# Optimization experiments

Hardware: AMD Instinct MI355X
Metric: run time of the kernel (lower is better)

## Reference

```python
import jax, jax.numpy as jnp
import numpy as np

B, S, E, D, H, L, V = 8, 128, 512, 1024, 16, 4, 32000
DH = D // H
FF = 4 * D
SCALE = 1.0 / (DH ** 0.5)
NEG = -1e30


def _layer_norm(x, g, b, eps=1e-5):
    m = jnp.mean(x, axis=-1, keepdims=True)
    v = jnp.mean((x - m) ** 2, axis=-1, keepdims=True)
    return (x - m) / jnp.sqrt(v + eps) * g + b


def _rel_shift(x):
    # x: [q, k, b, n] -> TransformerXL relative shift
    q, k, b, n = x.shape
    xp = jnp.concatenate([jnp.zeros((q, 1, b, n), x.dtype), x], axis=1)
    xp = xp.reshape(k + 1, q, b, n)
    return xp[1:].reshape(q, k, b, n)


def setup_inputs():
    key = jax.random.key(0)
    ks = jax.random.split(key, 40)
    g = lambda i, shape, s=0.02: jax.random.normal(ks[i], shape, jnp.float32) * s
    inp = {
        'input_ids': jax.random.randint(ks[0], (B, E), 0, V),
        'encoder_rep': jax.random.normal(ks[1], (B, E, D), jnp.float32),
        'input_mask': jnp.ones((B, E), jnp.float32),
        'decode_input': jax.random.randint(ks[2], (B, S), 0, V),
        'decode_target': jax.random.randint(ks[3], (B, S), 0, V),
        'word_emb': g(4, (V, D)),
        'qkv_w': g(5, (L, 3 * D, D)), 'r_w': g(6, (L, D, D)), 'o_w': g(7, (L, D, D)),
        'kv_w': g(8, (L, 2 * D, D)), 'q_w': g(9, (L, D, D)), 'io_w': g(10, (L, D, D)),
        'rr_bias': g(11, (L, H, DH)), 'rw_bias': g(12, (L, H, DH)),
        'ln1_g': jnp.ones((L, D)), 'ln1_b': jnp.zeros((L, D)),
        'ln2_g': jnp.ones((L, D)), 'ln2_b': jnp.zeros((L, D)),
        'ffn_w1': g(13, (L, FF, D)), 'ffn_b1': jnp.zeros((L, FF)),
        'ffn_w2': g(14, (L, D, FF)), 'ffn_b2': jnp.zeros((L, D)),
        'ln3_g': jnp.ones((L, D)), 'ln3_b': jnp.zeros((L, D)),
        'out_w': g(15, (D, D)), 'out_b': jnp.zeros((D,)),
        'copy_w': g(16, (D, D)), 'copy_b': jnp.zeros((D,)),
        'mode_w': g(17, (1, D)), 'mode_b': jnp.zeros((1,)),
    }
    return inp


def _forward(input_ids, encoder_rep, input_mask, decode_input, decode_target,
             word_emb, qkv_w, r_w, o_w, kv_w, q_w, io_w, rr_bias, rw_bias,
             ln1_g, ln1_b, ln2_g, ln2_b, ffn_w1, ffn_b1, ffn_w2, ffn_b2,
             ln3_g, ln3_b, out_w, out_b, copy_w, copy_b, mode_w, mode_b):
    # relative position embedding r: [S, D]
    pos_seq = jnp.arange(S - 1, -1, -1.0, dtype=jnp.float32)
    inv_freq = 1.0 / (10000.0 ** (jnp.arange(0.0, D, 2.0) / D))
    sin_inp = pos_seq[:, None] * inv_freq[None, :]
    r = jnp.concatenate([jnp.sin(sin_inp), jnp.cos(sin_inp)], axis=-1)

    causal = jnp.tril(jnp.ones((S, S), jnp.bool_))[:, :, None, None]  # [i,j,1,1]
    enc_mask_t = input_mask.T  # [E, B]

    core = word_emb[decode_input].transpose(1, 0, 2)  # [S, B, D]
    enc_t = encoder_rep.transpose(1, 0, 2)            # [E, B, D]

    for l in range(L):
        w = core
        heads = w @ qkv_w[l].T  # [S,B,3D]
        q, k, v = jnp.split(heads, 3, axis=-1)
        q = q.reshape(S, B, H, DH); k = k.reshape(S, B, H, DH); v = v.reshape(S, B, H, DH)
        r_k = (r @ r_w[l].T).reshape(S, H, DH)
        AC = jnp.einsum('ibnd,jbnd->ijbn', q + rw_bias[l], k)
        BD = _rel_shift(jnp.einsum('ibnd,jnd->ijbn', q + rr_bias[l], r_k))
        score = (AC + BD) * SCALE
        score = jnp.where(causal, score, NEG)
        prob = jax.nn.softmax(score, axis=1)
        vec = jnp.einsum('ijbn,jbnd->ibnd', prob, v).reshape(S, B, D)
        x = _layer_norm(w + vec @ o_w[l].T, ln1_g[l], ln1_b[l])

        # cross attention
        kv = enc_t @ kv_w[l].T
        k2, v2 = jnp.split(kv, 2, axis=-1)
        k2 = k2.reshape(E, B, H, DH); v2 = v2.reshape(E, B, H, DH)
        q2 = (x @ q_w[l].T).reshape(S, B, H, DH)
        score2 = jnp.einsum('qbnd,kbnd->qkbn', q2, k2) * SCALE
        score2 = score2 + (1.0 - enc_mask_t)[None, :, :, None] * NEG
        prob2 = jax.nn.softmax(score2, axis=1)
        vec2 = jnp.einsum('ijbn,jbnd->ibnd', prob2, v2).reshape(S, B, D)
        y = _layer_norm(x + vec2 @ io_w[l].T, ln2_g[l], ln2_b[l])

        # FFN (exact GELU as torch nn.GELU default)
        h = jax.nn.gelu(y @ ffn_w1[l].T + ffn_b1[l], approximate=False)
        h = h @ ffn_w2[l].T + ffn_b2[l]
        core = _layer_norm(y + h, ln3_g[l], ln3_b[l])

    core_out = core.transpose(1, 0, 2)  # [B, S, D]
    output = core_out @ out_w.T + out_b
    vocab_logits = output @ word_emb.T  # [B,S,V]
    vocab_prob = jax.nn.softmax(vocab_logits, axis=-1)

    copy_h = core_out @ copy_w.T + copy_b
    input_logits = jnp.einsum('bid,bjd->bij', copy_h, encoder_rep)
    input_logits = input_logits + (1.0 - input_mask[:, None, :]) * NEG
    input_prob = jax.nn.softmax(input_logits, axis=-1)  # [B,S,E]

    mode_sig = jax.nn.sigmoid(core_out @ mode_w.T + mode_b)  # [B,S,1]
    vocab_prob = vocab_prob * mode_sig

    idx = jnp.broadcast_to(input_ids[:, None, :], (B, S, E))
    b_i = jnp.arange(B)[:, None, None]
    s_i = jnp.arange(S)[None, :, None]
    vocab_prob = vocab_prob.at[b_i, s_i, idx].add((1.0 - mode_sig) * input_prob)

    flat = vocab_prob.reshape(-1, V)
    tgt = decode_target.reshape(-1)
    predict = jnp.take_along_axis(flat, tgt[:, None], axis=1)[:, 0]
    valid = (tgt != 0).astype(jnp.float32)
    loss = jnp.sum(-jnp.log(predict + 1e-6) * valid) / jnp.sum(valid)
    return jnp.repeat(loss[None], B)


def reference(input_ids, encoder_rep, input_mask, decode_input, decode_target,
              word_emb, qkv_w, r_w, o_w, kv_w, q_w, io_w, rr_bias, rw_bias,
              ln1_g, ln1_b, ln2_g, ln2_b, ffn_w1, ffn_b1, ffn_w2, ffn_b2,
              ln3_g, ln3_b, out_w, out_b, copy_w, copy_b, mode_w, mode_b):
    return _forward(input_ids, encoder_rep, input_mask, decode_input, decode_target,
                    word_emb, qkv_w, r_w, o_w, kv_w, q_w, io_w, rr_bias, rw_bias,
                    ln1_g, ln1_b, ln2_g, ln2_b, ffn_w1, ffn_b1, ffn_w2, ffn_b2,
                    ln3_g, ln3_b, out_w, out_b, copy_w, copy_b, mode_w, mode_b)
```

## Files before the change

kernel.cpp:

```cpp
#include <hip/hip_runtime.h>
#include <math.h>

#define B_ 8
#define S_ 128
#define E_ 512
#define D_ 1024
#define H_ 16
#define L_ 4
#define V_ 32000
#define DH_ 64
#define FF_ 4096
#define M_ 1024
#define ME_ 4096
#define NT_ 250
#define SCALE_F 0.125f
#define NEGV (-1e30f)

typedef __attribute__((ext_vector_type(8))) short short8;
typedef __attribute__((ext_vector_type(4))) float f32x4;

__device__ __forceinline__ float bf2f(ushort u) {
  union { unsigned int u32; float f; } v; v.u32 = ((unsigned int)u) << 16; return v.f;
}
__device__ __forceinline__ ushort f2bf(float x) {
  union { float f; unsigned int u; } v; v.f = x;
  unsigned int r = v.u + 0x7fff + ((v.u >> 16) & 1);
  return (ushort)(r >> 16);
}
__device__ __forceinline__ void gl_lds16(const ushort* g, ushort* l) {
  __builtin_amdgcn_global_load_lds((const __attribute__((address_space(1))) void*)g,
                                   (__attribute__((address_space(3))) void*)l, 16, 0, 0);
}

__device__ __forceinline__ float warp_reduce_sum(float v) {
#pragma unroll
  for (int o = 32; o > 0; o >>= 1) v += __shfl_down(v, o);
  return v;
}
__device__ __forceinline__ float warp_reduce_max(float v) {
#pragma unroll
  for (int o = 32; o > 0; o >>= 1) v = fmaxf(v, __shfl_down(v, o));
  return v;
}
__device__ __forceinline__ float block_reduce_sum(float v, float* sred) {
  v = warp_reduce_sum(v);
  __syncthreads();
  if ((threadIdx.x & 63) == 0) sred[threadIdx.x >> 6] = v;
  __syncthreads();
  float s = 0.0f;
  int nw = blockDim.x >> 6;
  for (int w = 0; w < nw; ++w) s += sred[w];
  return s;
}
__device__ __forceinline__ float block_reduce_max(float v, float* sred) {
  v = warp_reduce_max(v);
  __syncthreads();
  if ((threadIdx.x & 63) == 0) sred[threadIdx.x >> 6] = v;
  __syncthreads();
  float s = -3.4e38f;
  int nw = blockDim.x >> 6;
  for (int w = 0; w < nw; ++w) s = fmaxf(s, sred[w]);
  return s;
}

__global__ __launch_bounds__(256) void castf_kernel(const float* __restrict__ in,
                                                    ushort* __restrict__ out, int n4) {
  int t = blockIdx.x * 256 + threadIdx.x;
  if (t >= n4) return;
  float4 v = ((const float4*)in)[t];
  ushort4 o;
  o.x = f2bf(v.x); o.y = f2bf(v.y); o.z = f2bf(v.z); o.w = f2bf(v.w);
  ((ushort4*)out)[t] = o;
}

__global__ __launch_bounds__(256) void castlayer_kernel(
    const float* __restrict__ sqkv, const float* __restrict__ so,
    const float* __restrict__ sq, const float* __restrict__ sio,
    const float* __restrict__ sf1, const float* __restrict__ sf2,
    ushort* __restrict__ dqkv, ushort* __restrict__ dov,
    ushort* __restrict__ dq, ushort* __restrict__ dio,
    ushort* __restrict__ df1, ushort* __restrict__ df2) {
  int t = blockIdx.x * 256 + threadIdx.x;
  const float* src; ushort* dst; int idx;
  if (t < 786432)       { src = sqkv; dst = dqkv; idx = t; }
  else if (t < 1048576) { src = so;  dst = dov; idx = t - 786432; }
  else if (t < 1310720) { src = sq;  dst = dq;  idx = t - 1048576; }
  else if (t < 1572864) { src = sio; dst = dio; idx = t - 1310720; }
  else if (t < 2621440) { src = sf1; dst = df1; idx = t - 1572864; }
  else if (t < 3670016) { src = sf2; dst = df2; idx = t - 2621440; }
  else return;
  float4 v = ((const float4*)src)[idx];
  ushort4 o4;
  o4.x = f2bf(v.x); o4.y = f2bf(v.y); o4.z = f2bf(v.z); o4.w = f2bf(v.w);
  ((ushort4*)dst)[idx] = o4;
}

__global__ __launch_bounds__(256) void enct_kernel(const float* __restrict__ enc,
                                                   ushort* __restrict__ encT) {
  int t = blockIdx.x * 256 + threadIdx.x;
  if (t >= ME_ * D_) return;
  int d = t & (D_ - 1);
  int row = t >> 10;
  int e = row >> 3, b = row & 7;
  encT[t] = f2bf(enc[((size_t)b * E_ + e) * D_ + d]);
}

__global__ __launch_bounds__(256) void pos_emb_kernel(ushort* __restrict__ r) {
  int t = blockIdx.x * 256 + threadIdx.x;
  if (t >= S_ * D_) return;
  int i = t / D_, j = t % D_;
  float pos = (float)(S_ - 1 - i);
  int jj = (j < D_ / 2) ? j : (j - D_ / 2);
  float invf = powf(10000.0f, -(float)(2 * jj) / (float)D_);
  float a = pos * invf;
  r[t] = f2bf((j < D_ / 2) ? sinf(a) : cosf(a));
}

__global__ __launch_bounds__(256) void embed_kernel(const int* __restrict__ ids,
                                                    const float* __restrict__ emb,
                                                    float* __restrict__ core,
                                                    ushort* __restrict__ core_bf) {
  int t = blockIdx.x * 256 + threadIdx.x;
  if (t >= M_ * D_) return;
  int d = t & (D_ - 1);
  int row = t >> 10;
  int s = row >> 3, b = row & 7;
  float v = emb[(size_t)ids[b * S_ + s] * D_ + d];
  core[t] = v;
  core_bf[t] = f2bf(v);
}

template <int EPI>
__global__ __launch_bounds__(256) void gemm_w_kernel(
    const ushort* __restrict__ A, const ushort* __restrict__ Bm,
    const float* __restrict__ bias, void* __restrict__ Cv,
    int M, int N, int K, int ksplit,
    long long Arow, long long Abatch, long long Brow, long long Bbatch,
    long long Crow, long long Cbatch, long long Csplit) {
  __shared__ ushort lA[128 * 32];
  __shared__ ushort lB[128 * 32];
  int tid = threadIdx.x;
  int bz = blockIdx.z;
  int batch = bz / ksplit, split = bz % ksplit;
  int kLen = K / ksplit, kStart = split * kLen;
  const ushort* Ab = A + (size_t)batch * Abatch;
  const ushort* Bb = Bm + (size_t)batch * Bbatch;
  int bm = blockIdx.y * 128, bn = blockIdx.x * 128;
  int lane = tid & 63, wave = tid >> 6;
  int wrow = (wave >> 1) * 64, wcol = (wave & 1) * 64;
  int quad = lane >> 4, l16 = lane & 15;
  f32x4 acc[4][4];
#pragma unroll
  for (int i = 0; i < 4; ++i)
#pragma unroll
    for (int j = 0; j < 4; ++j) { acc[i][j][0] = 0.f; acc[i][j][1] = 0.f; acc[i][j][2] = 0.f; acc[i][j][3] = 0.f; }
  int r0 = tid >> 2, c0 = (tid & 3) * 8;
  int r1 = (tid + 256) >> 2;
  for (int k0 = kStart; k0 < kStart + kLen; k0 += 32) {
    __syncthreads();
    gl_lds16(Ab + (size_t)(bm + r0) * Arow + k0 + c0, &lA[(size_t)tid * 8]);
    gl_lds16(Ab + (size_t)(bm + r1) * Arow + k0 + c0, &lA[(size_t)(256 + tid) * 8]);
    gl_lds16(Bb + (size_t)(bn + r0) * Brow + k0 + c0, &lB[(size_t)tid * 8]);
    gl_lds16(Bb + (size_t)(bn + r1) * Brow + k0 + c0, &lB[(size_t)(256 + tid) * 8]);
    __syncthreads();
    short8 af[4], bfr[4];
#pragma unroll
    for (int mi = 0; mi < 4; ++mi)
      af[mi] = *(const short8*)&lA[(size_t)(wrow + mi * 16 + l16) * 32 + quad * 8];
#pragma unroll
    for (int ni = 0; ni < 4; ++ni)
      bfr[ni] = *(const short8*)&lB[(size_t)(wcol + ni * 16 + l16) * 32 + quad * 8];
#pragma unroll
    for (int mi = 0; mi < 4; ++mi)
#pragma unroll
      for (int ni = 0; ni < 4; ++ni)
        acc[mi][ni] = __builtin_amdgcn_mfma_f32_16x16x32_bf16(af[mi], bfr[ni], acc[mi][ni], 0, 0, 0);
  }
#pragma unroll
  for (int mi = 0; mi < 4; ++mi) {
    int row0 = bm + wrow + mi * 16 + quad * 4;
#pragma unroll
    for (int ni = 0; ni < 4; ++ni) {
      int col = bn + wcol + ni * 16 + l16;
      float bv = 0.f;
      if (EPI >= 3) bv = bias[col];
#pragma unroll
      for (int r = 0; r < 4; ++r) {
        float v = acc[mi][ni][r] + bv;
        if (EPI == 4) v = 0.5f * v * (1.0f + erff(v * 0.70710678118654752f));
        size_t ci = (size_t)split * Csplit + (size_t)batch * Cbatch + (size_t)(row0 + r) * Crow + col;
        if (EPI == 0) ((float*)Cv)[ci] = v;
        else ((ushort*)Cv)[ci] = f2bf(v);
      }
    }
  }
}

__global__ __launch_bounds__(256) void vocab_kernel(const ushort* __restrict__ A,
                                                    const ushort* __restrict__ Bm,
                                                    float* __restrict__ tmax,
                                                    float* __restrict__ tsum) {
  __shared__ ushort lA[128 * 32];
  __shared__ ushort lB[128 * 32];
  __shared__ float smax[2][128];
  __shared__ float ssum[2][128];
  int tid = threadIdx.x;
  int orig = blockIdx.x + gridDim.x * blockIdx.y;
  int wg = (orig & 7) * 250 + (orig >> 3);
  int bm = (wg & 7) * 128;
  int bnT = wg >> 3;
  int bn = bnT * 128;
  int lane = tid & 63, wave = tid >> 6;
  int wrow = (wave >> 1) * 64, half = wave & 1, wcol = half * 64;
  int quad = lane >> 4, l16 = lane & 15;
  f32x4 acc[4][4];
#pragma unroll
  for (int i = 0; i < 4; ++i)
#pragma unroll
    for (int j = 0; j < 4; ++j) { acc[i][j][0] = 0.f; acc[i][j][1] = 0.f; acc[i][j][2] = 0.f; acc[i][j][3] = 0.f; }
  int r0 = tid >> 2, c0 = (tid & 3) * 8;
  int r1 = (tid + 256) >> 2;
  for (int k0 = 0; k0 < D_; k0 += 32) {
    __syncthreads();
    gl_lds16(A + (size_t)(bm + r0) * 2048 + k0 + c0, &lA[(size_t)tid * 8]);
    gl_lds16(A + (size_t)(bm + r1) * 2048 + k0 + c0, &lA[(size_t)(256 + tid) * 8]);
    gl_lds16(Bm + (size_t)(bn + r0) * D_ + k0 + c0, &lB[(size_t)tid * 8]);
    gl_lds16(Bm + (size_t)(bn + r1) * D_ + k0 + c0, &lB[(size_t)(256 + tid) * 8]);
    __syncthreads();
    short8 af[4], bfr[4];
#pragma unroll
    for (int mi = 0; mi < 4; ++mi)
      af[mi] = *(const short8*)&lA[(size_t)(wrow + mi * 16 + l16) * 32 + quad * 8];
#pragma unroll
    for (int ni = 0; ni < 4; ++ni)
      bfr[ni] = *(const short8*)&lB[(size_t)(wcol + ni * 16 + l16) * 32 + quad * 8];
#pragma unroll
    for (int mi = 0; mi < 4; ++mi)
#pragma unroll
      for (int ni = 0; ni < 4; ++ni)
        acc[mi][ni] = __builtin_amdgcn_mfma_f32_16x16x32_bf16(af[mi], bfr[ni], acc[mi][ni], 0, 0, 0);
  }
#pragma unroll
  for (int mi = 0; mi < 4; ++mi)
#pragma unroll
    for (int r = 0; r < 4; ++r) {
      float lm = -3.4e38f;
#pragma unroll
      for (int ni = 0; ni < 4; ++ni) lm = fmaxf(lm, acc[mi][ni][r]);
#pragma unroll
      for (int o = 1; o < 16; o <<= 1) lm = fmaxf(lm, __shfl_xor(lm, o));
      if (l16 == 0) smax[half][wrow + mi * 16 + quad * 4 + r] = lm;
    }
  __syncthreads();
#pragma unroll
  for (int mi = 0; mi < 4; ++mi)
#pragma unroll
    for (int r = 0; r < 4; ++r) {
      int row = wrow + mi * 16 + quad * 4 + r;
      float m = fmaxf(smax[0][row], smax[1][row]);
      float ls = 0.f;
#pragma unroll
      for (int ni = 0; ni < 4; ++ni) ls += __expf(acc[mi][ni][r] - m);
#pragma unroll
      for (int o = 1; o < 16; o <<= 1) ls += __shfl_xor(ls, o);
      if (l16 == 0) ssum[half][row] = ls;
    }
  __syncthreads();
  if (tid < 128) {
    float m = fmaxf(smax[0][tid], smax[1][tid]);
    float s = ssum[0][tid] + ssum[1][tid];
    tmax[(size_t)(bm + tid) * NT_ + bnT] = m;
    tsum[(size_t)(bm + tid) * NT_ + bnT] = s;
  }
}

__global__ __launch_bounds__(256) void vocab_combine_kernel(const float* __restrict__ tmax,
                                                            const float* __restrict__ tsum,
                                                            float* __restrict__ rmax,
                                                            float* __restrict__ rsum) {
  __shared__ float sred[4];
  int m = blockIdx.x;
  float mx = -3.4e38f;
  for (int t = threadIdx.x; t < NT_; t += 256) mx = fmaxf(mx, tmax[(size_t)m * NT_ + t]);
  mx = block_reduce_max(mx, sred);
  float s = 0.f;
  for (int t = threadIdx.x; t < NT_; t += 256)
    s += tsum[(size_t)m * NT_ + t] * expf(tmax[(size_t)m * NT_ + t] - mx);
  s = block_reduce_sum(s, sred);
  if (threadIdx.x == 0) { rmax[m] = mx; rsum[m] = s; }
}

__global__ __launch_bounds__(256) void tlogit_kernel(const ushort* __restrict__ headout,
                                                     const ushort* __restrict__ emb,
                                                     const int* __restrict__ tgt,
                                                     float* __restrict__ tl) {
  __shared__ float sred[4];
  int m = blockIdx.x;
  int s = m >> 3, b = m & 7;
  int t = tgt[b * S_ + s];
  const ushort* a = headout + (size_t)m * 2048;
  const ushort* w = emb + (size_t)t * D_;
  float acc = 0.f;
  for (int i = threadIdx.x; i < D_; i += 256) acc += bf2f(a[i]) * bf2f(w[i]);
  acc = block_reduce_sum(acc, sred);
  if (threadIdx.x == 0) tl[m] = acc;
}

__global__ __launch_bounds__(256) void attn1_fused_kernel(const ushort* __restrict__ heads,
                                                          const ushort* __restrict__ rkproj,
                                                          const float* __restrict__ rw,
                                                          const float* __restrict__ rr,
                                                          ushort* __restrict__ attnA) {
  __shared__ float score[128][129];
  __shared__ ushort pP[128][136];
  __shared__ ushort vT[64][136];
  int bz = blockIdx.x;
  int b = bz >> 4, n = bz & 15;
  int tid = threadIdx.x, lane = tid & 63, wave = tid >> 6;
  int quad = lane >> 4, l16 = lane & 15;
  int wrow = wave * 32;

  {
    int j = tid >> 1, dbase = (tid & 1) * 32;
    const ushort* src = heads + (size_t)(j * 8 + b) * 3072 + 2048 + n * 64 + dbase;
#pragma unroll
    for (int c8 = 0; c8 < 4; ++c8) {
      short8 v8 = *(const short8*)(src + c8 * 8);
#pragma unroll
      for (int cc = 0; cc < 8; ++cc) vT[dbase + c8 * 8 + cc][j] = (ushort)v8[cc];
    }
  }

  short8 qrw[2][2], qrr[2][2];
#pragma unroll
  for (int mi = 0; mi < 2; ++mi) {
    int i = wrow + mi * 16 + l16;
    const ushort* qp = heads + (size_t)(i * 8 + b) * 3072 + n * 64;
#pragma unroll
    for (int kc = 0; kc < 2; ++kc) {
      int k0 = kc * 32 + quad * 8;
      short8 qv = *(const short8*)(qp + k0);
      short8 w, rv;
#pragma unroll
      for (int t = 0; t < 8; ++t) {
        float q = bf2f((ushort)qv[t]);
        w[t] = (short)f2bf(q + rw[n * 64 + k0 + t]);
        rv[t] = (short)f2bf(q + rr[n * 64 + k0 + t]);
      }
      qrw[mi][kc] = w; qrr[mi][kc] = rv;
    }
  }

  {
    f32x4 acc[2][8];
#pragma unroll
    for (int i = 0; i < 2; ++i)
#pragma unroll
      for (int j = 0; j < 8; ++j) { acc[i][j][0]=0.f; acc[i][j][1]=0.f; acc[i][j][2]=0.f; acc[i][j][3]=0.f; }
#pragma unroll
    for (int kc = 0; kc < 2; ++kc) {
      int k0 = kc * 32 + quad * 8;
      short8 kf[8];
#pragma unroll
      for (int ni = 0; ni < 8; ++ni) {
        int j = ni * 16 + l16;
        kf[ni] = *(const short8*)(heads + (size_t)(j * 8 + b) * 3072 + 1024 + n * 64 + k0);
      }
#pragma unroll
      for (int mi = 0; mi < 2; ++mi)
#pragma unroll
        for (int ni = 0; ni < 8; ++ni)
          acc[mi][ni] = __builtin_amdgcn_mfma_f32_16x16x32_bf16(qrw[mi][kc], kf[ni], acc[mi][ni], 0, 0, 0);
    }
#pragma unroll
    for (int mi = 0; mi < 2; ++mi)
#pragma unroll
      for (int ni = 0; ni < 8; ++ni)
#pragma unroll
        for (int r = 0; r < 4; ++r)
          score[wrow + mi * 16 + quad * 4 + r][ni * 16 + l16] = acc[mi][ni][r];
  }
  {
    f32x4 acc[2][8];
#pragma unroll
    for (int i = 0; i < 2; ++i)
#pragma unroll
      for (int j = 0; j < 8; ++j) { acc[i][j][0]=0.f; acc[i][j][1]=0.f; acc[i][j][2]=0.f; acc[i][j][3]=0.f; }
#pragma unroll
    for (int kc = 0; kc < 2; ++kc) {
      int k0 = kc * 32 + quad * 8;
      short8 rkf[8];
#pragma unroll
      for (int ni = 0; ni < 8; ++ni) {
        int jp = ni * 16 + l16;
        rkf[ni] = *(const short8*)(rkproj + (size_t)jp * 1024 + n * 64 + k0);
      }
#pragma unroll
      for (int mi = 0; mi < 2; ++mi)
#pragma unroll
        for (int ni = 0; ni < 8; ++ni)
          acc[mi][ni] = __builtin_amdgcn_mfma_f32_16x16x32_bf16(qrr[mi][kc], rkf[ni], acc[mi][ni], 0, 0, 0);
    }
#pragma unroll
    for (int mi = 0; mi < 2; ++mi)
#pragma unroll
      for (int r = 0; r < 4; ++r) {
        int i = wrow + mi * 16 + quad * 4 + r;
#pragma unroll
        for (int ni = 0; ni < 8; ++ni) {
          int jp = ni * 16 + l16;
          if (jp >= 127 - i) score[i][jp - 127 + i] += acc[mi][ni][r];
        }
      }
  }
  {
    int row = tid >> 1, halfc = (tid & 1) * 64;
    float mx = -3.4e38f;
    for (int c = halfc; c < halfc + 64; ++c) {
      float v = (c <= row) ? score[row][c] * SCALE_F : -3.4e38f;
      mx = fmaxf(mx, v);
    }
    mx = fmaxf(mx, __shfl_xor(mx, 1));
    float s = 0.f;
    for (int c = halfc; c < halfc + 64; ++c) {
      float e = (c <= row) ? __expf(score[row][c] * SCALE_F - mx) : 0.f;
      score[row][c] = e;
      s += e;
    }
    s += __shfl_xor(s, 1);
    float inv = 1.0f / s;
    for (int c = halfc; c < halfc + 64; ++c) pP[row][c] = f2bf(score[row][c] * inv);
  }
  __syncthreads();
  {
    f32x4 acc[2][4];
#pragma unroll
    for (int i = 0; i < 2; ++i)
#pragma unroll
      for (int j = 0; j < 4; ++j) { acc[i][j][0]=0.f; acc[i][j][1]=0.f; acc[i][j][2]=0.f; acc[i][j][3]=0.f; }
#pragma unroll
    for (int kc = 0; kc < 4; ++kc) {
      int k0 = kc * 32 + quad * 8;
      short8 pf[2], vf[4];
#pragma unroll
      for (int mi = 0; mi < 2; ++mi)
        pf[mi] = *(const short8*)&pP[wrow + mi * 16 + l16][k0];
#pragma unroll
      for (int ni = 0; ni < 4; ++ni)
        vf[ni] = *(const short8*)&vT[ni * 16 + l16][k0];
#pragma unroll
      for (int mi = 0; mi < 2; ++mi)
#pragma unroll
        for (int ni = 0; ni < 4; ++ni)
          acc[mi][ni] = __builtin_amdgcn_mfma_f32_16x16x32_bf16(pf[mi], vf[ni], acc[mi][ni], 0, 0, 0);
    }
#pragma unroll
    for (int mi = 0; mi < 2; ++mi)
#pragma unroll
      for (int r = 0; r < 4; ++r) {
        int i = wrow + mi * 16 + quad * 4 + r;
#pragma unroll
        for (int ni = 0; ni < 4; ++ni)
          attnA[(size_t)(i * 8 + b) * 1024 + n * 64 + ni * 16 + l16] = f2bf(acc[mi][ni][r]);
      }
  }
}

__global__ __launch_bounds__(256) void attn2_fused_kernel(const float* __restrict__ q0,
                                                          const float* __restrict__ q1,
                                                          const ushort* __restrict__ kvproj,
                                                          const float* __restrict__ mask,
                                                          ushort* __restrict__ attnA) {
  __shared__ ushort vT[64][136];
  __shared__ ushort pP[128][136];
  __shared__ float mtile[128];
  int bz = blockIdx.x;
  int b = bz >> 4, n = bz & 15;
  int tid = threadIdx.x, lane = tid & 63, wave = tid >> 6;
  int quad = lane >> 4, l16 = lane & 15;
  int wrow = wave * 32;
  short8 qf[2][2];
#pragma unroll
  for (int mi = 0; mi < 2; ++mi) {
    int i = wrow + mi * 16 + l16;
    size_t base = (size_t)(i * 8 + b) * 1024 + n * 64;
#pragma unroll
    for (int kc = 0; kc < 2; ++kc) {
      int k0 = kc * 32 + quad * 8;
      short8 v;
#pragma unroll
      for (int t = 0; t < 8; ++t) v[t] = (short)f2bf(q0[base + k0 + t] + q1[base + k0 + t]);
      qf[mi][kc] = v;
    }
  }
  float m_run[2][4], l_run[2][4];
#pragma unroll
  for (int mi = 0; mi < 2; ++mi)
#pragma unroll
    for (int r = 0; r < 4; ++r) { m_run[mi][r] = -3.0e38f; l_run[mi][r] = 0.f; }
  f32x4 accO[2][4];
#pragma unroll
  for (int i = 0; i < 2; ++i)
#pragma unroll
    for (int j = 0; j < 4; ++j) { accO[i][j][0]=0.f; accO[i][j][1]=0.f; accO[i][j][2]=0.f; accO[i][j][3]=0.f; }

  for (int et = 0; et < 4; ++et) {
    __syncthreads();
    {
      int j = tid >> 1, dbase = (tid & 1) * 32;
      int e = et * 128 + j;
      const ushort* src = kvproj + (size_t)(e * 8 + b) * 2048 + 1024 + n * 64 + dbase;
#pragma unroll
      for (int c8 = 0; c8 < 4; ++c8) {
        short8 v8 = *(const short8*)(src + c8 * 8);
#pragma unroll
        for (int cc = 0; cc < 8; ++cc) vT[dbase + c8 * 8 + cc][j] = (ushort)v8[cc];
      }
      if (tid < 128) mtile[tid] = (1.0f - mask[b * E_ + et * 128 + tid]) * NEGV;
    }
    f32x4 accS[2][8];
#pragma unroll
    for (int i = 0; i < 2; ++i)
#pragma unroll
      for (int j = 0; j < 8; ++j) { accS[i][j][0]=0.f; accS[i][j][1]=0.f; accS[i][j][2]=0.f; accS[i][j][3]=0.f; }
#pragma unroll
    for (int kc = 0; kc < 2; ++kc) {
      int k0 = kc * 32 + quad * 8;
      short8 kf[8];
#pragma unroll
      for (int ni = 0; ni < 8; ++ni) {
        int e = et * 128 + ni * 16 + l16;
        kf[ni] = *(const short8*)(kvproj + (size_t)(e * 8 + b) * 2048 + n * 64 + k0);
      }
#pragma unroll
      for (int mi = 0; mi < 2; ++mi)
#pragma unroll
        for (int ni = 0; ni < 8; ++ni)
          accS[mi][ni] = __builtin_amdgcn_mfma_f32_16x16x32_bf16(qf[mi][kc], kf[ni], accS[mi][ni], 0, 0, 0);
    }
    __syncthreads();
#pragma unroll
    for (int mi = 0; mi < 2; ++mi)
#pragma unroll
      for (int r = 0; r < 4; ++r) {
        float v[8];
        float vmax = -3.4e38f;
#pragma unroll
        for (int ni = 0; ni < 8; ++ni) {
          v[ni] = accS[mi][ni][r] * SCALE_F + mtile[ni * 16 + l16];
          vmax = fmaxf(vmax, v[ni]);
        }
#pragma unroll
        for (int o = 1; o < 16; o <<= 1) vmax = fmaxf(vmax, __shfl_xor(vmax, o));
        float mnew = fmaxf(m_run[mi][r], vmax);
        float alpha = __expf(m_run[mi][r] - mnew);
        float ls = 0.f;
        int row = wrow + mi * 16 + quad * 4 + r;
#pragma unroll
        for (int ni = 0; ni < 8; ++ni) {
          float p = __expf(v[ni] - mnew);
          ls += p;
          pP[row][ni * 16 + l16] = f2bf(p);
        }
#pragma unroll
        for (int o = 1; o < 16; o <<= 1) ls += __shfl_xor(ls, o);
        l_run[mi][r] = l_run[mi][r] * alpha + ls;
        m_run[mi][r] = mnew;
#pragma unroll
        for (int ni = 0; ni < 4; ++ni) accO[mi][ni][r] *= alpha;
      }
#pragma unroll
    for (int kc = 0; kc < 4; ++kc) {
      int k0 = kc * 32 + quad * 8;
      short8 pf[2], vf[4];
#pragma unroll
      for (int mi = 0; mi < 2; ++mi)
        pf[mi] = *(const short8*)&pP[wrow + mi * 16 + l16][k0];
#pragma unroll
      for (int ni = 0; ni < 4; ++ni)
        vf[ni] = *(const short8*)&vT[ni * 16 + l16][k0];
#pragma unroll
      for (int mi = 0; mi < 2; ++mi)
#pragma unroll
        for (int ni = 0; ni < 4; ++ni)
          accO[mi][ni] = __builtin_amdgcn_mfma_f32_16x16x32_bf16(pf[mi], vf[ni], accO[mi][ni], 0, 0, 0);
    }
  }
#pragma unroll
  for (int mi = 0; mi < 2; ++mi)
#pragma unroll
    for (int r = 0; r < 4; ++r) {
      int i = wrow + mi * 16 + quad * 4 + r;
      float inv = 1.0f / l_run[mi][r];
#pragma unroll
      for (int ni = 0; ni < 4; ++ni)
        attnA[(size_t)(i * 8 + b) * 1024 + n * 64 + ni * 16 + l16] = f2bf(accO[mi][ni][r] * inv);
    }
}

__global__ __launch_bounds__(256) void addln_kernel(const float* __restrict__ a,
                                                    const float* __restrict__ c,
                                                    int nsplit, long long cstride,
                                                    const float* __restrict__ bias,
                                                    const float* __restrict__ g,
                                                    const float* __restrict__ bb,
                                                    float* __restrict__ out,
                                                    ushort* __restrict__ out_bf) {
  __shared__ float sred[4];
  int row = blockIdx.x;
  const float* pa = a + (size_t)row * D_;
  float vals[4];
  float s = 0.f;
#pragma unroll
  for (int it = 0; it < 4; ++it) {
    int idx = threadIdx.x + it * 256;
    float v = pa[idx];
    for (int sp = 0; sp < nsplit; ++sp) v += c[(size_t)sp * cstride + (size_t)row * D_ + idx];
    if (bias) v += bias[idx];
    vals[it] = v;
    s += v;
  }
  s = block_reduce_sum(s, sred);
  float mean = s * (1.0f / D_);
  float ss = 0.f;
#pragma unroll
  for (int it = 0; it < 4; ++it) {
    float dd = vals[it] - mean;
    ss += dd * dd;
  }
  ss = block_reduce_sum(ss, sred);
  float inv = rsqrtf(ss * (1.0f / D_) + 1e-5f);
#pragma unroll
  for (int it = 0; it < 4; ++it) {
    int idx = threadIdx.x + it * 256;
    float r = (vals[it] - mean) * inv * g[idx] + bb[idx];
    out[(size_t)row * D_ + idx] = r;
    out_bf[(size_t)row * D_ + idx] = f2bf(r);
  }
}

__global__ __launch_bounds__(256) void mode_kernel(const float* __restrict__ core,
                                                   const float* __restrict__ mode_w,
                                                   const float* __restrict__ mode_b,
                                                   float* __restrict__ mode_sig) {
  __shared__ float sred[4];
  int m = blockIdx.x;
  const float* a = core + (size_t)m * D_;
  float s = 0.f;
  for (int t = threadIdx.x; t < D_; t += 256) s += a[t] * mode_w[t];
  s = block_reduce_sum(s, sred);
  if (threadIdx.x == 0) mode_sig[m] = 1.0f / (1.0f + expf(-(s + mode_b[0])));
}

__global__ __launch_bounds__(256) void final_kernel(const float* __restrict__ lg,
                                                    const int* __restrict__ ids,
                                                    const float* __restrict__ mask,
                                                    const int* __restrict__ tgt,
                                                    const float* __restrict__ mode_sig,
                                                    const float* __restrict__ tlogit,
                                                    const float* __restrict__ rmax,
                                                    const float* __restrict__ rsum,
                                                    float* __restrict__ loss_acc) {
  __shared__ float sred[4];
  int s = blockIdx.x, b = blockIdx.y;
  int m = s * B_ + b;
  size_t base = (size_t)(b * S_ + s) * E_;
  const long long LGS = (long long)B_ * S_ * E_;
  int tg = tgt[b * S_ + s];
  float lv[2];
  float mx = -3.4e38f;
#pragma unroll
  for (int it = 0; it < 2; ++it) {
    int e = threadIdx.x + it * 256;
    float raw = 0.f;
#pragma unroll
    for (int sp = 0; sp < 4; ++sp) raw += lg[sp * LGS + base + e];
    raw += (1.0f - mask[b * E_ + e]) * NEGV;
    lv[it] = raw;
    mx = fmaxf(mx, raw);
  }
  mx = block_reduce_max(mx, sred);
  float ssum = 0.f, csum = 0.f;
#pragma unroll
  for (int it = 0; it < 2; ++it) {
    int e = threadIdx.x + it * 256;
    float ev = expf(lv[it] - mx);
    ssum += ev;
    if (ids[b * E_ + e] == tg) csum += ev;
  }
  ssum = block_reduce_sum(ssum, sred);
  csum = block_reduce_sum(csum, sred);
  if (threadIdx.x == 0) {
    float copy_p = csum / ssum;
    float pv = expf(tlogit[m] - rmax[m]) / rsum[m];
    float msig = mode_sig[m];
    float predict = pv * msig + (1.0f - msig) * copy_p;
    float valid = (tg != 0) ? 1.0f : 0.0f;
    atomicAdd(&loss_acc[0], -logf(predict + 1e-6f) * valid);
    atomicAdd(&loss_acc[1], valid);
  }
}

__global__ void writeout_kernel(const float* __restrict__ loss_acc, float* __restrict__ out) {
  if (threadIdx.x < B_) out[threadIdx.x] = loss_acc[0] / loss_acc[1];
}

static void gw(hipStream_t st, int epi, const ushort* A, const ushort* B, const float* bias,
               void* C, int M, int N, int K,
               long long Ar, long long Ab, long long Br, long long Bb,
               long long Cr, long long Cb, int nb, int ksplit, long long Csplit) {
  dim3 g(N / 128, M / 128, nb * ksplit);
  switch (epi) {
    case 0: gemm_w_kernel<0><<<g, 256, 0, st>>>(A, B, bias, C, M, N, K, ksplit, Ar, Ab, Br, Bb, Cr, Cb, Csplit); break;
    case 1: gemm_w_kernel<1><<<g, 256, 0, st>>>(A, B, bias, C, M, N, K, ksplit, Ar, Ab, Br, Bb, Cr, Cb, Csplit); break;
    case 3: gemm_w_kernel<3><<<g, 256, 0, st>>>(A, B, bias, C, M, N, K, ksplit, Ar, Ab, Br, Bb, Cr, Cb, Csplit); break;
    case 4: gemm_w_kernel<4><<<g, 256, 0, st>>>(A, B, bias, C, M, N, K, ksplit, Ar, Ab, Br, Bb, Cr, Cb, Csplit); break;
  }
}
static void castTo(hipStream_t st, const float* src, ushort* dst, size_t count) {
  int n4 = (int)(count / 4);
  castf_kernel<<<(n4 + 255) / 256, 256, 0, st>>>(src, dst, n4);
}

extern "C" void kernel_launch(void* const* d_in, const int* in_sizes, int n_in,
                              void* d_out, int out_size, void* d_ws, size_t ws_size,
                              hipStream_t stream) {
  const int* input_ids = (const int*)d_in[0];
  const float* encoder_rep = (const float*)d_in[1];
  const float* input_mask = (const float*)d_in[2];
  const int* decode_input = (const int*)d_in[3];
  const int* decode_target = (const int*)d_in[4];
  const float* word_emb = (const float*)d_in[5];
  const float* qkv_w = (const float*)d_in[6];
  const float* r_w = (const float*)d_in[7];
  const float* o_w = (const float*)d_in[8];
  const float* kv_w = (const float*)d_in[9];
  const float* q_w = (const float*)d_in[10];
  const float* io_w = (const float*)d_in[11];
  const float* rr_bias = (const float*)d_in[12];
  const float* rw_bias = (const float*)d_in[13];
  const float* ln1_g = (const float*)d_in[14];
  const float* ln1_b = (const float*)d_in[15];
  const float* ln2_g = (const float*)d_in[16];
  const float* ln2_b = (const float*)d_in[17];
  const float* ffn_w1 = (const float*)d_in[18];
  const float* ffn_b1 = (const float*)d_in[19];
  const float* ffn_w2 = (const float*)d_in[20];
  const float* ffn_b2 = (const float*)d_in[21];
  const float* ln3_g = (const float*)d_in[22];
  const float* ln3_b = (const float*)d_in[23];
  const float* out_w = (const float*)d_in[24];
  const float* out_b = (const float*)d_in[25];
  const float* copy_w = (const float*)d_in[26];
  const float* copy_b = (const float*)d_in[27];
  const float* mode_w = (const float*)d_in[28];
  const float* mode_b = (const float*)d_in[29];
  float* out = (float*)d_out;

  char* base = (char*)d_ws;
  size_t off = 0;
  auto alloc = [&](size_t bytes) -> void* {
    void* p = base + off;
    off = (off + bytes + 255) & ~(size_t)255;
    return p;
  };

  ushort* wl_qkv = (ushort*)alloc((size_t)3 * D_ * D_ * 2);
  ushort* wl_o = (ushort*)alloc((size_t)D_ * D_ * 2);
  ushort* wl_q = (ushort*)alloc((size_t)D_ * D_ * 2);
  ushort* wl_io = (ushort*)alloc((size_t)D_ * D_ * 2);
  ushort* wl_f1 = (ushort*)alloc((size_t)FF_ * D_ * 2);
  ushort* wl_f2 = (ushort*)alloc((size_t)FF_ * D_ * 2);
  ushort* wl_kv = (ushort*)alloc((size_t)L_ * 2 * D_ * D_ * 2);
  ushort* wl_r = (ushort*)alloc((size_t)L_ * D_ * D_ * 2);
  ushort* kvproj_bf = (ushort*)alloc((size_t)L_ * ME_ * 2 * D_ * 2);
  ushort* rkproj_bf = (ushort*)alloc((size_t)L_ * S_ * D_ * 2);

  ushort* w_emb = (ushort*)alloc((size_t)V_ * D_ * 2);
  ushort* w_oc = (ushort*)alloc((size_t)2048 * D_ * 2);
  float* b_oc = (float*)alloc(2048 * 4);
  ushort* enc_bf = (ushort*)alloc((size_t)ME_ * D_ * 2);
  ushort* encT_bf = (ushort*)alloc((size_t)ME_ * D_ * 2);
  ushort* r_bf = (ushort*)alloc((size_t)S_ * D_ * 2);
  float* f_core = (float*)alloc((size_t)M_ * D_ * 4);
  ushort* core_bf = (ushort*)alloc((size_t)M_ * D_ * 2);
  ushort* heads_bf = (ushort*)alloc((size_t)M_ * 3 * D_ * 2);
  ushort* attnA_bf = (ushort*)alloc((size_t)M_ * D_ * 2);
  float* f_tmp = (float*)alloc((size_t)4 * M_ * D_ * 4);
  float* f_x = (float*)alloc((size_t)M_ * D_ * 4);
  ushort* x_bf = (ushort*)alloc((size_t)M_ * D_ * 2);
  float* f_y = (float*)alloc((size_t)M_ * D_ * 4);
  ushort* y_bf = (ushort*)alloc((size_t)M_ * D_ * 2);
  float* f_q = (float*)alloc((size_t)2 * M_ * D_ * 4);
  ushort* ffnh_bf = (ushort*)alloc((size_t)M_ * FF_ * 2);
  ushort* headout_bf = (ushort*)alloc((size_t)M_ * 2048 * 2);
  float* f_lg = (float*)alloc((size_t)4 * B_ * S_ * E_ * 4);
  float* f_tmax = (float*)alloc((size_t)M_ * NT_ * 4);
  float* f_tsum = (float*)alloc((size_t)M_ * NT_ * 4);
  float* f_rmax = (float*)alloc(M_ * 4);
  float* f_rsum = (float*)alloc(M_ * 4);
  float* f_tlogit = (float*)alloc(M_ * 4);
  float* f_mode = (float*)alloc(M_ * 4);
  float* f_loss = (float*)alloc(64);

  castTo(stream, word_emb, w_emb, (size_t)V_ * D_);
  castTo(stream, out_w, w_oc, (size_t)D_ * D_);
  castTo(stream, copy_w, w_oc + (size_t)D_ * D_, (size_t)D_ * D_);
  hipMemcpyAsync(b_oc, out_b, D_ * 4, hipMemcpyDeviceToDevice, stream);
  hipMemcpyAsync(b_oc + D_, copy_b, D_ * 4, hipMemcpyDeviceToDevice, stream);
  castTo(stream, encoder_rep, enc_bf, (size_t)ME_ * D_);
  enct_kernel<<<(ME_ * D_) / 256, 256, 0, stream>>>(encoder_rep, encT_bf);
  pos_emb_kernel<<<(S_ * D_ + 255) / 256, 256, 0, stream>>>(r_bf);
  embed_kernel<<<(M_ * D_) / 256, 256, 0, stream>>>(decode_input, word_emb, f_core, core_bf);

  castTo(stream, kv_w, wl_kv, (size_t)L_ * 2 * D_ * D_);
  castTo(stream, r_w, wl_r, (size_t)L_ * D_ * D_);
  gw(stream, 1, encT_bf, wl_kv, nullptr, kvproj_bf, ME_, 2 * D_, D_,
     D_, 0, D_, (long long)2 * D_ * D_, 2 * D_, (long long)ME_ * 2 * D_, L_, 1, 0);
  gw(stream, 1, r_bf, wl_r, nullptr, rkproj_bf, S_, D_, D_,
     D_, 0, D_, (long long)D_ * D_, D_, (long long)S_ * D_, L_, 1, 0);

  for (int l = 0; l < L_; ++l) {
    castlayer_kernel<<<14336, 256, 0, stream>>>(
        qkv_w + (size_t)l * 3 * D_ * D_, o_w + (size_t)l * D_ * D_,
        q_w + (size_t)l * D_ * D_, io_w + (size_t)l * D_ * D_,
        ffn_w1 + (size_t)l * FF_ * D_, ffn_w2 + (size_t)l * FF_ * D_,
        wl_qkv, wl_o, wl_q, wl_io, wl_f1, wl_f2);

    gw(stream, 1, core_bf, wl_qkv, nullptr, heads_bf, M_, 3 * D_, D_, D_, 0, D_, 0, 3 * D_, 0, 1, 1, 0);
    attn1_fused_kernel<<<B_ * H_, 256, 0, stream>>>(heads_bf, rkproj_bf + (size_t)l * S_ * D_,
                                                    rw_bias + (size_t)l * D_,
                                                    rr_bias + (size_t)l * D_, attnA_bf);
    gw(stream, 0, attnA_bf, wl_o, nullptr, f_tmp, M_, D_, D_, D_, 0, D_, 0, D_, 0, 1, 2,
       (long long)M_ * D_);
    addln_kernel<<<M_, 256, 0, stream>>>(f_core, f_tmp, 2, (long long)M_ * D_, nullptr,
                                         ln1_g + (size_t)l * D_, ln1_b + (size_t)l * D_, f_x, x_bf);

    gw(stream, 0, x_bf, wl_q, nullptr, f_q, M_, D_, D_, D_, 0, D_, 0, D_, 0, 1, 2,
       (long long)M_ * D_);
    attn2_fused_kernel<<<B_ * H_, 256, 0, stream>>>(f_q, f_q + (size_t)M_ * D_,
                                                    kvproj_bf + (size_t)l * ME_ * 2 * D_,
                                                    input_mask, attnA_bf);
    gw(stream, 0, attnA_bf, wl_io, nullptr, f_tmp, M_, D_, D_, D_, 0, D_, 0, D_, 0, 1, 2,
       (long long)M_ * D_);
    addln_kernel<<<M_, 256, 0, stream>>>(f_x, f_tmp, 2, (long long)M_ * D_, nullptr,
                                         ln2_g + (size_t)l * D_, ln2_b + (size_t)l * D_, f_y, y_bf);

    gw(stream, 4, y_bf, wl_f1, ffn_b1 + (size_t)l * FF_, ffnh_bf, M_, FF_, D_, D_, 0, D_, 0, FF_, 0, 1, 1, 0);
    gw(stream, 0, ffnh_bf, wl_f2, nullptr, f_tmp, M_, D_, FF_, FF_, 0, FF_, 0, D_, 0, 1, 4,
       (long long)M_ * D_);
    addln_kernel<<<M_, 256, 0, stream>>>(f_y, f_tmp, 4, (long long)M_ * D_,
                                         ffn_b2 + (size_t)l * D_,
                                         ln3_g + (size_t)l * D_, ln3_b + (size_t)l * D_, f_core, core_bf);
  }

  gw(stream, 3, core_bf, w_oc, b_oc, headout_bf, M_, 2048, D_, D_, 0, D_, 0, 2048, 0, 1, 1, 0);
  mode_kernel<<<M_, 256, 0, stream>>>(f_core, mode_w, mode_b, f_mode);

  vocab_kernel<<<dim3(M_ / 128, V_ / 128), 256, 0, stream>>>(headout_bf, w_emb, f_tmax, f_tsum);
  vocab_combine_kernel<<<M_, 256, 0, stream>>>(f_tmax, f_tsum, f_rmax, f_rsum);
  tlogit_kernel<<<M_, 256, 0, stream>>>(headout_bf, w_emb, decode_target, f_tlogit);

  gw(stream, 0, headout_bf + D_, enc_bf, nullptr, f_lg, S_, E_, D_,
     (long long)B_ * 2048, 2048, D_, (long long)E_ * D_, E_, (long long)S_ * E_, B_, 4,
     (long long)B_ * S_ * E_);

  hipMemsetAsync(f_loss, 0, 2 * sizeof(float), stream);
  final_kernel<<<dim3(S_, B_), 256, 0, stream>>>(f_lg, input_ids, input_mask, decode_target,
                                                 f_mode, f_tlogit, f_rmax, f_rsum, f_loss);
  writeout_kernel<<<1, 64, 0, stream>>>(f_loss, out);
}
```

Measured before the change: 1.614 ms.

## Replace vocab and KV-projection GEMMs with pipelined 256x256 tile kernel

```diff
diff --git a/kernel.cpp b/kernel.cpp
--- a/kernel.cpp
+++ b/kernel.cpp
@@ -12,7 +12,7 @@
 #define FF_ 4096
 #define M_ 1024
 #define ME_ 4096
-#define NT_ 250
+#define NT_ 125
 #define SCALE_F 0.125f
 #define NEGV (-1e30f)
 
@@ -196,81 +196,156 @@
   }
 }
 
-__global__ __launch_bounds__(256) void vocab_kernel(const ushort* __restrict__ A,
-                                                    const ushort* __restrict__ Bm,
-                                                    float* __restrict__ tmax,
-                                                    float* __restrict__ tsum) {
-  __shared__ ushort lA[128 * 32];
-  __shared__ ushort lB[128 * 32];
-  __shared__ float smax[2][128];
-  __shared__ float ssum[2][128];
+template <int EPI>
+__global__ __launch_bounds__(512, 2) void gemm256_kernel(
+    const ushort* __restrict__ A, const ushort* __restrict__ Bm, void* __restrict__ Cv,
+    float* __restrict__ tmax, float* __restrict__ tsum,
+    long long Arow, long long Abatch, long long Brow, long long Bbatch,
+    long long Crow, long long Cbatch) {
+  __shared__ ushort sT[4][2][2][128 * 32];
+  __shared__ float smax[256][4];
+  __shared__ float ssum[256][4];
+  const int NK = 32;
   int tid = threadIdx.x;
-  int orig = blockIdx.x + gridDim.x * blockIdx.y;
-  int wg = (orig & 7) * 250 + (orig >> 3);
-  int bm = (wg & 7) * 128;
-  int bnT = wg >> 3;
-  int bn = bnT * 128;
+  int bm, bn, bnT = 0, batch = 0;
+  if constexpr (EPI == 5) {
+    int orig = blockIdx.x;
+    int xcd = orig & 7;
+    int base = (xcd < 4) ? xcd * 63 : 4 * 63 + (xcd - 4) * 62;
+    int wg = base + (orig >> 3);
+    bm = (wg & 3) * 256;
+    bnT = wg >> 2;
+    bn = bnT * 256;
+  } else {
+    bn = blockIdx.x * 256;
+    bm = blockIdx.y * 256;
+    batch = blockIdx.z;
+  }
+  const ushort* Ab = A + (size_t)batch * Abatch;
+  const ushort* Bb = Bm + (size_t)batch * Bbatch;
   int lane = tid & 63, wave = tid >> 6;
-  int wrow = (wave >> 1) * 64, half = wave & 1, wcol = half * 64;
+  int wr = wave >> 2;
+  int wc = wave & 3;
+  int bhalf = wc >> 1;
+  int brow0 = (wc & 1) * 64;
   int quad = lane >> 4, l16 = lane & 15;
-  f32x4 acc[4][4];
-#pragma unroll
-  for (int i = 0; i < 4; ++i)
-#pragma unroll
-    for (int j = 0; j < 4; ++j) { acc[i][j][0] = 0.f; acc[i][j][1] = 0.f; acc[i][j][2] = 0.f; acc[i][j][3] = 0.f; }
-  int r0 = tid >> 2, c0 = (tid & 3) * 8;
-  int r1 = (tid + 256) >> 2;
-  for (int k0 = 0; k0 < D_; k0 += 32) {
+  int sr = tid >> 2, sc = (tid & 3) * 8;
+
+  f32x4 acc[8][4];
+#pragma unroll
+  for (int i = 0; i < 8; ++i)
+#pragma unroll
+    for (int j = 0; j < 4; ++j) { acc[i][j][0]=0.f; acc[i][j][1]=0.f; acc[i][j][2]=0.f; acc[i][j][3]=0.f; }
+
+#define STAGE_HALF(s_, ab_, h_)                                                        \
+  do {                                                                                 \
+    int s__ = (s_); int b__ = s__ & 3;                                                 \
+    if ((ab_) == 0)                                                                    \
+      gl_lds16(Ab + (size_t)(bm + (h_) * 128 + sr) * Arow + s__ * 32 + sc,             \
+               &sT[b__][0][h_][tid * 8]);                                              \
+    else                                                                               \
+      gl_lds16(Bb + (size_t)(bn + (h_) * 128 + sr) * Brow + s__ * 32 + sc,             \
+               &sT[b__][1][h_][tid * 8]);                                              \
+  } while (0)
+
+#pragma unroll
+  for (int s = 0; s < 3; ++s) {
+    STAGE_HALF(s, 0, 0); STAGE_HALF(s, 0, 1);
+    STAGE_HALF(s, 1, 0); STAGE_HALF(s, 1, 1);
+  }
+  asm volatile("s_waitcnt vmcnt(8)");
+  __builtin_amdgcn_s_barrier();
+  __builtin_amdgcn_sched_barrier(0);
+
+  short8 af[4], bfv[4];
+  for (int t = 0; t < NK; ++t) {
+    int bt = t & 3;
+#pragma unroll
+    for (int i = 0; i < 4; ++i)
+      af[i] = *(const short8*)&sT[bt][0][wr][(i * 16 + l16) * 32 + quad * 8];
+#pragma unroll
+    for (int i = 0; i < 4; ++i)
+      bfv[i] = *(const short8*)&sT[bt][1][bhalf][(brow0 + i * 16 + l16) * 32 + quad * 8];
+    if (t + 3 < NK) { STAGE_HALF(t + 3, 0, 0); STAGE_HALF(t + 3, 0, 1); }
+    __builtin_amdgcn_s_barrier();
+    __builtin_amdgcn_sched_barrier(0);
+    __builtin_amdgcn_s_setprio(1);
+#pragma unroll
+    for (int mi = 0; mi < 4; ++mi)
+#pragma unroll
+      for (int ni = 0; ni < 4; ++ni)
+        acc[mi][ni] = __builtin_amdgcn_mfma_f32_16x16x32_bf16(af[mi], bfv[ni], acc[mi][ni], 0, 0, 0);
+    __builtin_amdgcn_s_setprio(0);
+    __builtin_amdgcn_s_barrier();
+    __builtin_amdgcn_sched_barrier(0);
+#pragma unroll
+    for (int i = 0; i < 4; ++i)
+      af[i] = *(const short8*)&sT[bt][0][wr][((4 + i) * 16 + l16) * 32 + quad * 8];
+    if (t + 3 < NK) { STAGE_HALF(t + 3, 1, 0); STAGE_HALF(t + 3, 1, 1); }
+    if (t + 3 < NK)      asm volatile("s_waitcnt vmcnt(8)");
+    else if (t + 2 < NK) asm volatile("s_waitcnt vmcnt(4)");
+    else                 asm volatile("s_waitcnt vmcnt(0)");
+    __builtin_amdgcn_s_barrier();
+    __builtin_amdgcn_sched_barrier(0);
+    __builtin_amdgcn_s_setprio(1);
+#pragma unroll
+    for (int mi = 0; mi < 4; ++mi)
+#pragma unroll
+      for (int ni = 0; ni < 4; ++ni)
+        acc[4 + mi][ni] = __builtin_amdgcn_mfma_f32_16x16x32_bf16(af[mi], bfv[ni], acc[4 + mi][ni], 0, 0, 0);
+    __builtin_amdgcn_s_setprio(0);
+    __builtin_amdgcn_s_barrier();
+    __builtin_amdgcn_sched_barrier(0);
+  }
+#undef STAGE_HALF
+
+  if constexpr (EPI == 5) {
+#pragma unroll
+    for (int mi = 0; mi < 8; ++mi)
+#pragma unroll
+      for (int r = 0; r < 4; ++r) {
+        int rr = wr * 128 + mi * 16 + quad * 4 + r;
+        float lm = -3.4e38f;
+#pragma unroll
+        for (int ni = 0; ni < 4; ++ni) lm = fmaxf(lm, acc[mi][ni][r]);
+#pragma unroll
+        for (int o = 1; o < 16; o <<= 1) lm = fmaxf(lm, __shfl_xor(lm, o));
+        if (l16 == 0) smax[rr][wc] = lm;
+      }
     __syncthreads();
-    gl_lds16(A + (size_t)(bm + r0) * 2048 + k0 + c0, &lA[(size_t)tid * 8]);
-    gl_lds16(A + (size_t)(bm + r1) * 2048 + k0 + c0, &lA[(size_t)(256 + tid) * 8]);
-    gl_lds16(Bm + (size_t)(bn + r0) * D_ + k0 + c0, &lB[(size_t)tid * 8]);
-    gl_lds16(Bm + (size_t)(bn + r1) * D_ + k0 + c0, &lB[(size_t)(256 + tid) * 8]);
+#pragma unroll
+    for (int mi = 0; mi < 8; ++mi)
+#pragma unroll
+      for (int r = 0; r < 4; ++r) {
+        int rr = wr * 128 + mi * 16 + quad * 4 + r;
+        float m = fmaxf(fmaxf(smax[rr][0], smax[rr][1]), fmaxf(smax[rr][2], smax[rr][3]));
+        float ls = 0.f;
+#pragma unroll
+        for (int ni = 0; ni < 4; ++ni) ls += __expf(acc[mi][ni][r] - m);
+#pragma unroll
+        for (int o = 1; o < 16; o <<= 1) ls += __shfl_xor(ls, o);
+        if (l16 == 0) ssum[rr][wc] = ls;
+      }
     __syncthreads();
-    short8 af[4], bfr[4];
-#pragma unroll
-    for (int mi = 0; mi < 4; ++mi)
-      af[mi] = *(const short8*)&lA[(size_t)(wrow + mi * 16 + l16) * 32 + quad * 8];
-#pragma unroll
-    for (int ni = 0; ni < 4; ++ni)
-      bfr[ni] = *(const short8*)&lB[(size_t)(wcol + ni * 16 + l16) * 32 + quad * 8];
-#pragma unroll
-    for (int mi = 0; mi < 4; ++mi)
-#pragma unroll
-      for (int ni = 0; ni < 4; ++ni)
-        acc[mi][ni] = __builtin_amdgcn_mfma_f32_16x16x32_bf16(af[mi], bfr[ni], acc[mi][ni], 0, 0, 0);
-  }
-#pragma unroll
-  for (int mi = 0; mi < 4; ++mi)
-#pragma unroll
-    for (int r = 0; r < 4; ++r) {
-      float lm = -3.4e38f;
-#pragma unroll
-      for (int ni = 0; ni < 4; ++ni) lm = fmaxf(lm, acc[mi][ni][r]);
-#pragma unroll
-      for (int o = 1; o < 16; o <<= 1) lm = fmaxf(lm, __shfl_xor(lm, o));
-      if (l16 == 0) smax[half][wrow + mi * 16 + quad * 4 + r] = lm;
-    }
-  __syncthreads();
-#pragma unroll
-  for (int mi = 0; mi < 4; ++mi)
-#pragma unroll
-    for (int r = 0; r < 4; ++r) {
-      int row = wrow + mi * 16 + quad * 4 + r;
-      float m = fmaxf(smax[0][row], smax[1][row]);
-      float ls = 0.f;
-#pragma unroll
-      for (int ni = 0; ni < 4; ++ni) ls += __expf(acc[mi][ni][r] - m);
-#pragma unroll
-      for (int o = 1; o < 16; o <<= 1) ls += __shfl_xor(ls, o);
-      if (l16 == 0) ssum[half][row] = ls;
-    }
-  __syncthreads();
-  if (tid < 128) {
-    float m = fmaxf(smax[0][tid], smax[1][tid]);
-    float s = ssum[0][tid] + ssum[1][tid];
-    tmax[(size_t)(bm + tid) * NT_ + bnT] = m;
-    tsum[(size_t)(bm + tid) * NT_ + bnT] = s;
+    if (tid < 256) {
+      float m = fmaxf(fmaxf(smax[tid][0], smax[tid][1]), fmaxf(smax[tid][2], smax[tid][3]));
+      float s = ssum[tid][0] + ssum[tid][1] + ssum[tid][2] + ssum[tid][3];
+      tmax[(size_t)(bm + tid) * NT_ + bnT] = m;
+      tsum[(size_t)(bm + tid) * NT_ + bnT] = s;
+    }
+  } else {
+    ushort* C = (ushort*)Cv + (size_t)batch * Cbatch;
+#pragma unroll
+    for (int mi = 0; mi < 8; ++mi) {
+      int row0 = bm + wr * 128 + mi * 16 + quad * 4;
+#pragma unroll
+      for (int ni = 0; ni < 4; ++ni) {
+        int col = bn + wc * 64 + ni * 16 + l16;
+#pragma unroll
+        for (int r = 0; r < 4; ++r)
+          C[(size_t)(row0 + r) * Crow + col] = f2bf(acc[mi][ni][r]);
+      }
+    }
   }
 }
 
@@ -815,8 +890,9 @@
 
   castTo(stream, kv_w, wl_kv, (size_t)L_ * 2 * D_ * D_);
   castTo(stream, r_w, wl_r, (size_t)L_ * D_ * D_);
-  gw(stream, 1, encT_bf, wl_kv, nullptr, kvproj_bf, ME_, 2 * D_, D_,
-     D_, 0, D_, (long long)2 * D_ * D_, 2 * D_, (long long)ME_ * 2 * D_, L_, 1, 0);
+  gemm256_kernel<1><<<dim3(2 * D_ / 256, ME_ / 256, L_), 512, 0, stream>>>(
+      encT_bf, wl_kv, kvproj_bf, nullptr, nullptr,
+      D_, 0, D_, (long long)2 * D_ * D_, 2 * D_, (long long)ME_ * 2 * D_);
   gw(stream, 1, r_bf, wl_r, nullptr, rkproj_bf, S_, D_, D_,
      D_, 0, D_, (long long)D_ * D_, D_, (long long)S_ * D_, L_, 1, 0);
 
@@ -857,7 +933,8 @@
   gw(stream, 3, core_bf, w_oc, b_oc, headout_bf, M_, 2048, D_, D_, 0, D_, 0, 2048, 0, 1, 1, 0);
   mode_kernel<<<M_, 256, 0, stream>>>(f_core, mode_w, mode_b, f_mode);
 
-  vocab_kernel<<<dim3(M_ / 128, V_ / 128), 256, 0, stream>>>(headout_bf, w_emb, f_tmax, f_tsum);
+  gemm256_kernel<5><<<500, 512, 0, stream>>>(headout_bf, w_emb, nullptr, f_tmax, f_tsum,
+                                             2048, 0, D_, 0, 0, 0);
   vocab_combine_kernel<<<M_, 256, 0, stream>>>(f_tmax, f_tsum, f_rmax, f_rsum);
   tlogit_kernel<<<M_, 256, 0, stream>>>(headout_bf, w_emb, decode_target, f_tlogit);
 
```

After: 1.588 ms. Within noise of the previous version (-1.6%).
